# Kernel tuning notes

Measured on AMD Instinct MI355X. Metric: run time of the kernel, lower is better.

## Reference

```python
import jax, jax.numpy as jnp
import numpy as np

N_MLPS = 256
N_BLOCKS = 8
TCODE = 13
IN_F = 3
HID = 128
OUT_F = 1
B = 256
NPTS = 2048
K = 256  # 8-bit codebook
OMEGA = 30.0

# per-layer (fan_in, fan_out) for weight reconstruction
LAYER_SHAPES = [(IN_F + TCODE, HID), (HID, HID), (HID, HID), (HID, OUT_F)]


def setup_inputs() -> dict:
    key = jax.random.key(0)
    ks = jax.random.split(key, 20)
    inp = {
        "x": jax.random.uniform(ks[0], (B, NPTS, IN_F), jnp.float32, -1.0, 1.0),
        "mlp_idx": jax.random.randint(ks[1], (B,), 0, N_MLPS, jnp.int32),
        "block_idx": jax.random.randint(ks[2], (B,), 0, N_BLOCKS, jnp.int32),
        "latent_table": jax.random.normal(ks[3], (N_MLPS, N_BLOCKS, TCODE), jnp.float32),
    }
    for l, (fi, fo) in enumerate(LAYER_SHAPES):
        bound = 1.0 / np.sqrt(fi)
        inp[f"centroids_l{l}"] = jax.random.uniform(ks[4 + 3 * l], (K,), jnp.float32, -bound, bound)
        inp[f"labels_l{l}"] = jax.random.randint(ks[5 + 3 * l], (N_MLPS * fi * fo,), 0, K, jnp.int32)
        inp[f"bias_l{l}"] = jax.random.uniform(ks[6 + 3 * l], (N_MLPS, 1, fo), jnp.float32, -bound, bound)
    return inp


def _layer(h, idx, centroids, labels, bias, fi, fo, apply_sin):
    # codebook dequant: weight.view(-1)[:] = centroids[labels]
    weight = centroids[labels].reshape(N_MLPS, fi, fo)
    # indexed bmm: torch.bmm(x, weight[indices]) + bias[indices]
    out = jnp.einsum("bni,bio->bno", h, weight[idx]) + bias[idx]
    return jnp.sin(OMEGA * out) if apply_sin else out


def reference(x, mlp_idx, block_idx, latent_table,
              centroids_l0, labels_l0, bias_l0,
              centroids_l1, labels_l1, bias_l1,
              centroids_l2, labels_l2, bias_l2,
              centroids_l3, labels_l3, bias_l3):
    # gather per-sample latent code and concat with coords
    z = latent_table[mlp_idx, block_idx]                      # [B, TCODE]
    h = jnp.concatenate(
        [x, jnp.broadcast_to(z[:, None, :], (x.shape[0], x.shape[1], TCODE))], axis=-1)
    cs = [centroids_l0, centroids_l1, centroids_l2, centroids_l3]
    ls = [labels_l0, labels_l1, labels_l2, labels_l3]
    bs = [bias_l0, bias_l1, bias_l2, bias_l3]
    for l, (fi, fo) in enumerate(LAYER_SHAPES):
        h = _layer(h, mlp_idx, cs[l], ls[l], bs[l], fi, fo, apply_sin=(l < len(LAYER_SHAPES) - 1))
    return h
```

## Files before the change

### kernel.cpp

```cpp
#include <hip/hip_runtime.h>


typedef unsigned int u32;
typedef unsigned short u16;
typedef __bf16 v8bf  __attribute__((ext_vector_type(8)));
typedef __bf16 v2bf  __attribute__((ext_vector_type(2)));
typedef float  v16f  __attribute__((ext_vector_type(16)));
typedef float  v2f   __attribute__((ext_vector_type(2)));
typedef u32    v4u   __attribute__((ext_vector_type(4)));
typedef u32    v2u   __attribute__((ext_vector_type(2)));

#define MFMA(a, b, c) __builtin_amdgcn_mfma_f32_32x32x16_bf16(a, b, c, 0, 0, 0)

#define HSTRIDE 136
#define OMEGA_S 4.774648292756860f

__device__ __forceinline__ float sinrev(float rev) {
    return __builtin_amdgcn_sinf(__builtin_amdgcn_fractf(rev));
}

__device__ __forceinline__ u32 pack2(float c) {
    __bf16 b0 = (__bf16)c;
    float  f0 = (float)b0;
    __bf16 b1 = (__bf16)(c - f0);
    return (u32)__builtin_bit_cast(u16, b0) |
           ((u32)__builtin_bit_cast(u16, b1) << 16);
}

__device__ __forceinline__ void pk2(float s0, float s1, u32& lo, u32& hi) {
    v2f s; s[0] = s0; s[1] = s1;
    v2bf l = __builtin_convertvector(s, v2bf);
    u32 lov = __builtin_bit_cast(u32, l);
    v2f lf;
    lf[0] = __builtin_bit_cast(float, lov << 16);
    lf[1] = __builtin_bit_cast(float, lov & 0xffff0000u);
    v2f r = s - lf;
    v2bf h = __builtin_convertvector(r, v2bf);
    lo = lov;
    hi = __builtin_bit_cast(u32, h);
}

__device__ __forceinline__ u32 pklo(float s0, float s1) {
    v2f s; s[0] = s0; s[1] = s1;
    v2bf l = __builtin_convertvector(s, v2bf);
    return __builtin_bit_cast(u32, l);
}

#define PLO(a, b) __builtin_amdgcn_perm((a), (b), 0x05040100u)
#define PHI(a, b) __builtin_amdgcn_perm((a), (b), 0x07060302u)

__global__ __launch_bounds__(512)
void ecnr_dequant(const float* __restrict__ cent0, const int* __restrict__ lab0,
                  const float* __restrict__ cent1, const int* __restrict__ lab1,
                  const float* __restrict__ cent2, const int* __restrict__ lab2,
                  const float* __restrict__ cent3, const int* __restrict__ lab3,
                  const float* __restrict__ bias0, const float* __restrict__ bias1,
                  const float* __restrict__ bias2,
                  u16* __restrict__ wpl1, u16* __restrict__ wpl2,
                  u16* __restrict__ w0pl, u16* __restrict__ w3pl,
                  float* __restrict__ biasc)
{
    __shared__ u32 cpk[512];
    const int t = threadIdx.x;

    if (blockIdx.x < 512) {
        const int m = blockIdx.x >> 1, L = blockIdx.x & 1;
        if (t < 256) cpk[t] = pack2((L ? cent2 : cent1)[t] * OMEGA_S);
        __syncthreads();
        const int* lab = (L ? lab2 : lab1) + (size_t)m * 16384;
        u16* base = (L ? wpl2 : wpl1) + (size_t)m * 32768;
        #pragma unroll
        for (int i = 0; i < 4; ++i) {
            const int id = i * 512 + t;
            const int n = id & 127, c = id >> 7;
            u32 g[8];
            #pragma unroll
            for (int j = 0; j < 8; ++j) g[j] = cpk[lab[(8 * c + j) * 128 + n]];
            v4u lo, hi;
            #pragma unroll
            for (int r = 0; r < 4; ++r) {
                lo[r] = PLO(g[2 * r + 1], g[2 * r]);
                hi[r] = PHI(g[2 * r + 1], g[2 * r]);
            }
            *(v4u*)(base + c * 1024 + n * 8)         = lo;
            *(v4u*)(base + 16384 + c * 1024 + n * 8) = hi;
        }
    } else {
        const int m = blockIdx.x - 512;
        if (t < 256) cpk[t] = pack2(cent0[t] * OMEGA_S);
        else         cpk[t] = pack2(cent3[t - 256]);
        __syncthreads();
        if (t < 256) {
            const int n = t & 127, c = t >> 7;
            const int* lab = lab0 + (size_t)m * 2048;
            u32 g[8];
            #pragma unroll
            for (int j = 0; j < 8; ++j) g[j] = cpk[lab[(8 * c + j) * 128 + n]];
            v4u lo, hi;
            #pragma unroll
            for (int r = 0; r < 4; ++r) {
                lo[r] = PLO(g[2 * r + 1], g[2 * r]);
                hi[r] = PHI(g[2 * r + 1], g[2 * r]);
            }
            u16* b0 = w0pl + (size_t)m * 4096;
            *(v4u*)(b0 + c * 1024 + n * 8)        = lo;
            *(v4u*)(b0 + 2048 + c * 1024 + n * 8) = hi;
        } else if (t < 384) {
            const int kk = t - 256;
            const u32 u = cpk[256 + lab3[(size_t)m * 128 + kk]];
            w3pl[(size_t)m * 256 + kk]       = (u16)u;
            w3pl[(size_t)m * 256 + 128 + kk] = (u16)(u >> 16);
        }
        if (t < 384) {
            const int li = t >> 7, kk = t & 127;
            const float* bsrc = (li == 0) ? bias0 : (li == 1) ? bias1 : bias2;
            biasc[(size_t)m * 384 + t] = bsrc[m * 128 + kk] * OMEGA_S;
        }
    }
}

__global__ __launch_bounds__(512, 8)
void ecnr_fwd(const float* __restrict__ x,
              const int*   __restrict__ mlp_idx,
              const int*   __restrict__ block_idx,
              const float* __restrict__ latent,
              const float* __restrict__ bias3,
              const u16* __restrict__ wpl1, const u16* __restrict__ wpl2,
              const u16* __restrict__ w0pl, const u16* __restrict__ w3pl,
              const float* __restrict__ biasc,
              float* __restrict__ out)
{
    __shared__ __attribute__((aligned(16))) u16   Hlo[64 * HSTRIDE];
    __shared__ __attribute__((aligned(16))) u16   Hhi[64 * HSTRIDE];
    __shared__ __attribute__((aligned(16))) float biasS[2 * 128];
    __shared__ __attribute__((aligned(16))) float red[2 * 128];

    const int g    = blockIdx.x;
    const int b    = ((g >> 8) << 3) | (g & 7);
    const int p0   = ((g >> 3) & 31) * 64;
    const int m    = mlp_idx[b];

    const int t  = threadIdx.x;
    const int l  = t & 63, w = t >> 6;
    const int q  = l >> 5, ln = l & 31;
    const int pt = w & 1, nt = w >> 1;
    const int mrow = pt * 32 + ln;
    const int nn   = nt * 32 + ln;
    const int bidx = nt * 32 + 4 * q;

    const float* bc = biasc + (size_t)m * 384;
    if (t < 128) {
        biasS[t]       = bc[128 + t];
        biasS[128 + t] = bc[256 + t];
    }
    const float* xp = x + (size_t)(b * 2048 + p0 + mrow) * 3;
    const float xv0 = xp[0], xv1 = xp[1], xv2 = xp[2];
    const u16* w0p = w0pl + (size_t)m * 4096 + q * 1024 + nn * 8;
    const v4u w0lo = *(const v4u*)(w0p);
    const v4u w0hi = *(const v4u*)(w0p + 2048);
    float4 b0f[4];
    #pragma unroll
    for (int gg = 0; gg < 4; ++gg)
        b0f[gg] = *(const float4*)(bc + bidx + 8 * gg);
    const float* zp = latent + ((size_t)m * 8 + block_idx[b]) * 13;
    float zr[8];
    #pragma unroll
    for (int j = 0; j < 8; ++j) zr[j] = zp[q * 5 + j];

    u16* lop = Hlo + mrow * HSTRIDE + nt * 32 + 4 * q;
    u16* hip = Hhi + mrow * HSTRIDE + nt * 32 + 4 * q;

    {
        float fin[8];
        if (q == 0) {
            fin[0] = xv0; fin[1] = xv1; fin[2] = xv2;
            #pragma unroll
            for (int j = 0; j < 5; ++j) fin[3 + j] = zr[j];
        } else {
            #pragma unroll
            for (int j = 0; j < 8; ++j) fin[j] = zr[j];
        }
        v4u il, ih;
        #pragma unroll
        for (int r = 0; r < 4; ++r) {
            u32 plo, phi;
            pk2(fin[2 * r], fin[2 * r + 1], plo, phi);
            il[r] = plo; ih[r] = phi;
        }
        const v8bf inlo = __builtin_bit_cast(v8bf, il);
        const v8bf inhi = __builtin_bit_cast(v8bf, ih);
        const v8bf wl = __builtin_bit_cast(v8bf, w0lo);
        const v8bf wh = __builtin_bit_cast(v8bf, w0hi);
        v16f acc;
        #pragma unroll
        for (int gg = 0; gg < 4; ++gg) {
            acc[4 * gg] = b0f[gg].x; acc[4 * gg + 1] = b0f[gg].y;
            acc[4 * gg + 2] = b0f[gg].z; acc[4 * gg + 3] = b0f[gg].w;
        }
        acc = MFMA(wl, inlo, acc);
        acc = MFMA(wl, inhi, acc);
        acc = MFMA(wh, inlo, acc);
        #pragma unroll
        for (int gg = 0; gg < 4; ++gg) {
            const float s0 = sinrev(acc[4 * gg + 0]);
            const float s1 = sinrev(acc[4 * gg + 1]);
            const float s2 = sinrev(acc[4 * gg + 2]);
            const float s3 = sinrev(acc[4 * gg + 3]);
            u32 l0, h0, l1, h1;
            pk2(s0, s1, l0, h0);
            pk2(s2, s3, l1, h1);
            v2u lov, hiv;
            lov[0] = l0; lov[1] = l1;
            hiv[0] = h0; hiv[1] = h1;
            *(v2u*)(lop + 8 * gg) = lov;
            *(v2u*)(hip + 8 * gg) = hiv;
        }
    }
    __syncthreads();

    const u16* HLO = Hlo + mrow * HSTRIDE + q * 8;
    const u16* HHI = Hhi + mrow * HSTRIDE + q * 8;
    #pragma unroll 1
    for (int L = 0; L < 2; ++L) {
        const u16* Wb = (L ? wpl2 : wpl1) + (size_t)m * 32768 + q * 1024 + nn * 8;
        v16f acc;
        #pragma unroll
        for (int gg = 0; gg < 4; ++gg) {
            const float4 bv = *(const float4*)&biasS[L * 128 + bidx + 8 * gg];
            acc[4 * gg] = bv.x; acc[4 * gg + 1] = bv.y;
            acc[4 * gg + 2] = bv.z; acc[4 * gg + 3] = bv.w;
        }
        v4u wl8[8];
        #pragma unroll
        for (int kc = 0; kc < 8; ++kc)
            wl8[kc] = *(const v4u*)(Wb + kc * 2048);
        #pragma unroll
        for (int kc = 0; kc < 8; ++kc) {
            const v4u whv = *(const v4u*)(Wb + kc * 2048 + 16384);
            const v8bf hlo = *(const v8bf*)(HLO + kc * 16);
            const v8bf hhi = *(const v8bf*)(HHI + kc * 16);
            acc = MFMA(__builtin_bit_cast(v8bf, wl8[kc]), hlo, acc);
            acc = MFMA(__builtin_bit_cast(v8bf, wl8[kc]), hhi, acc);
            acc = MFMA(__builtin_bit_cast(v8bf, whv), hlo, acc);
        }
        __syncthreads();
        if (L == 0) {
            #pragma unroll
            for (int gg = 0; gg < 4; ++gg) {
                const float s0 = sinrev(acc[4 * gg + 0]);
                const float s1 = sinrev(acc[4 * gg + 1]);
                const float s2 = sinrev(acc[4 * gg + 2]);
                const float s3 = sinrev(acc[4 * gg + 3]);
                u32 l0, h0, l1, h1;
                pk2(s0, s1, l0, h0);
                pk2(s2, s3, l1, h1);
                v2u lov, hiv;
                lov[0] = l0; lov[1] = l1;
                hiv[0] = h0; hiv[1] = h1;
                *(v2u*)(lop + 8 * gg) = lov;
                *(v2u*)(hip + 8 * gg) = hiv;
            }
        } else {
            #pragma unroll
            for (int gg = 0; gg < 4; ++gg) {
                const float s0 = sinrev(acc[4 * gg + 0]);
                const float s1 = sinrev(acc[4 * gg + 1]);
                const float s2 = sinrev(acc[4 * gg + 2]);
                const float s3 = sinrev(acc[4 * gg + 3]);
                v2u lov;
                lov[0] = pklo(s0, s1);
                lov[1] = pklo(s2, s3);
                *(v2u*)(lop + 8 * gg) = lov;
            }
        }
        __syncthreads();
    }

    {
        const u16* w3b = w3pl + (size_t)m * 256 + nt * 32 + q * 8;
        const u16* h3l = Hlo + mrow * HSTRIDE + nt * 32 + q * 8;
        v16f a3;
        #pragma unroll
        for (int r = 0; r < 16; ++r) a3[r] = 0.0f;
        #pragma unroll
        for (int kc = 0; kc < 2; ++kc) {
            const v8bf wl = *(const v8bf*)(w3b + kc * 16);
            const v8bf wh = *(const v8bf*)(w3b + 128 + kc * 16);
            const v8bf hl = *(const v8bf*)(h3l + kc * 16);
            a3 = MFMA(wl, hl, a3);
            a3 = MFMA(wh, hl, a3);
        }
        if (q == 0) red[pt * 128 + nt * 32 + ln] = a3[0];
    }
    __syncthreads();

    if (t < 64) {
        const int rp = (t >> 5) * 128, rl = t & 31;
        const float o = bias3[m]
            + red[rp + rl] + red[rp + 32 + rl]
            + red[rp + 64 + rl] + red[rp + 96 + rl];
        out[(size_t)b * 2048 + p0 + t] = o;
    }
}

extern "C" void kernel_launch(void* const* d_in, const int* in_sizes, int n_in,
                              void* d_out, int out_size, void* d_ws, size_t ws_size,
                              hipStream_t stream) {
    (void)in_sizes; (void)n_in; (void)out_size; (void)ws_size;
    u16*   wpl1  = (u16*)d_ws;
    u16*   wpl2  = wpl1 + (size_t)256 * 32768;
    u16*   w0pl  = wpl2 + (size_t)256 * 32768;
    u16*   w3pl  = w0pl + (size_t)256 * 4096;
    float* biasc = (float*)(w3pl + (size_t)256 * 256);

    ecnr_dequant<<<768, 512, 0, stream>>>(
        (const float*)d_in[4],  (const int*)d_in[5],
        (const float*)d_in[7],  (const int*)d_in[8],
        (const float*)d_in[10], (const int*)d_in[11],
        (const float*)d_in[13], (const int*)d_in[14],
        (const float*)d_in[6],  (const float*)d_in[9], (const float*)d_in[12],
        wpl1, wpl2, w0pl, w3pl, biasc);

    ecnr_fwd<<<8192, 512, 0, stream>>>(
        (const float*)d_in[0], (const int*)d_in[1], (const int*)d_in[2],
        (const float*)d_in[3],
        (const float*)d_in[15],
        wpl1, wpl2, w0pl, w3pl, biasc,
        (float*)d_out);
}
```

Before: 241.3 us.

## Halve block to 4 waves, each computing two 32-point tiles per weight load

Each wave now handles both 32-row point tiles (A and B) for its 32 output columns, so every weight fragment loaded from global memory feeds two MFMA chains instead of one. The block shrinks from 512 to 256 threads, which halves redundant weight loads per block and interleaves two independent accumulator chains to hide MFMA latency. s_setprio is raised around the MFMA bursts. The cost is roughly double the accumulator and input registers per thread and fewer waves per block, which may reduce occupancy.

```diff
diff --git a/kernel.cpp b/kernel.cpp
--- a/kernel.cpp
+++ b/kernel.cpp
@@ -119,7 +119,42 @@
     }
 }
 
-__global__ __launch_bounds__(512, 8)
+
+#define EPI_FULL(ACC, LOP, HIP)                                   \
+    do {                                                          \
+        _Pragma("unroll")                                         \
+        for (int gg = 0; gg < 4; ++gg) {                          \
+            const float s0 = sinrev((ACC)[4 * gg + 0]);           \
+            const float s1 = sinrev((ACC)[4 * gg + 1]);           \
+            const float s2 = sinrev((ACC)[4 * gg + 2]);           \
+            const float s3 = sinrev((ACC)[4 * gg + 3]);           \
+            u32 l0, h0, l1, h1;                                   \
+            pk2(s0, s1, l0, h0);                                  \
+            pk2(s2, s3, l1, h1);                                  \
+            v2u lov, hiv;                                         \
+            lov[0] = l0; lov[1] = l1;                             \
+            hiv[0] = h0; hiv[1] = h1;                             \
+            *(v2u*)((LOP) + 8 * gg) = lov;                        \
+            *(v2u*)((HIP) + 8 * gg) = hiv;                        \
+        }                                                         \
+    } while (0)
+
+#define EPI_LO(ACC, LOP)                                          \
+    do {                                                          \
+        _Pragma("unroll")                                         \
+        for (int gg = 0; gg < 4; ++gg) {                          \
+            const float s0 = sinrev((ACC)[4 * gg + 0]);           \
+            const float s1 = sinrev((ACC)[4 * gg + 1]);           \
+            const float s2 = sinrev((ACC)[4 * gg + 2]);           \
+            const float s3 = sinrev((ACC)[4 * gg + 3]);           \
+            v2u lov;                                              \
+            lov[0] = pklo(s0, s1);                                \
+            lov[1] = pklo(s2, s3);                                \
+            *(v2u*)((LOP) + 8 * gg) = lov;                        \
+        }                                                         \
+    } while (0)
+
+__global__ __launch_bounds__(256, 4)
 void ecnr_fwd(const float* __restrict__ x,
               const int*   __restrict__ mlp_idx,
               const int*   __restrict__ block_idx,
@@ -141,10 +176,8 @@
     const int m    = mlp_idx[b];
 
     const int t  = threadIdx.x;
-    const int l  = t & 63, w = t >> 6;
+    const int l  = t & 63, nt = t >> 6;
     const int q  = l >> 5, ln = l & 31;
-    const int pt = w & 1, nt = w >> 1;
-    const int mrow = pt * 32 + ln;
     const int nn   = nt * 32 + ln;
     const int bidx = nt * 32 + 4 * q;
 
@@ -153,8 +186,9 @@
         biasS[t]       = bc[128 + t];
         biasS[128 + t] = bc[256 + t];
     }
-    const float* xp = x + (size_t)(b * 2048 + p0 + mrow) * 3;
-    const float xv0 = xp[0], xv1 = xp[1], xv2 = xp[2];
+    const float* xpA = x + (size_t)(b * 2048 + p0 + ln) * 3;
+    const float xA0 = xpA[0], xA1 = xpA[1], xA2 = xpA[2];
+    const float xB0 = xpA[96], xB1 = xpA[97], xB2 = xpA[98];
     const u16* w0p = w0pl + (size_t)m * 4096 + q * 1024 + nn * 8;
     const v4u w0lo = *(const v4u*)(w0p);
     const v4u w0hi = *(const v4u*)(w0p + 2048);
@@ -167,68 +201,70 @@
     #pragma unroll
     for (int j = 0; j < 8; ++j) zr[j] = zp[q * 5 + j];
 
-    u16* lop = Hlo + mrow * HSTRIDE + nt * 32 + 4 * q;
-    u16* hip = Hhi + mrow * HSTRIDE + nt * 32 + 4 * q;
+    u16* lopA = Hlo + ln * HSTRIDE + nt * 32 + 4 * q;
+    u16* hipA = Hhi + ln * HSTRIDE + nt * 32 + 4 * q;
+    u16* lopB = lopA + 32 * HSTRIDE;
+    u16* hipB = hipA + 32 * HSTRIDE;
 
     {
-        float fin[8];
+        float finA[8], finB[8];
         if (q == 0) {
-            fin[0] = xv0; fin[1] = xv1; fin[2] = xv2;
-            #pragma unroll
-            for (int j = 0; j < 5; ++j) fin[3 + j] = zr[j];
+            finA[0] = xA0; finA[1] = xA1; finA[2] = xA2;
+            finB[0] = xB0; finB[1] = xB1; finB[2] = xB2;
+            #pragma unroll
+            for (int j = 0; j < 5; ++j) { finA[3 + j] = zr[j]; finB[3 + j] = zr[j]; }
         } else {
             #pragma unroll
-            for (int j = 0; j < 8; ++j) fin[j] = zr[j];
-        }
-        v4u il, ih;
+            for (int j = 0; j < 8; ++j) { finA[j] = zr[j]; finB[j] = zr[j]; }
+        }
+        v4u ilA, ihA, ilB, ihB;
         #pragma unroll
         for (int r = 0; r < 4; ++r) {
             u32 plo, phi;
-            pk2(fin[2 * r], fin[2 * r + 1], plo, phi);
-            il[r] = plo; ih[r] = phi;
-        }
-        const v8bf inlo = __builtin_bit_cast(v8bf, il);
-        const v8bf inhi = __builtin_bit_cast(v8bf, ih);
+            pk2(finA[2 * r], finA[2 * r + 1], plo, phi);
+            ilA[r] = plo; ihA[r] = phi;
+            pk2(finB[2 * r], finB[2 * r + 1], plo, phi);
+            ilB[r] = plo; ihB[r] = phi;
+        }
+        const v8bf inloA = __builtin_bit_cast(v8bf, ilA);
+        const v8bf inhiA = __builtin_bit_cast(v8bf, ihA);
+        const v8bf inloB = __builtin_bit_cast(v8bf, ilB);
+        const v8bf inhiB = __builtin_bit_cast(v8bf, ihB);
         const v8bf wl = __builtin_bit_cast(v8bf, w0lo);
         const v8bf wh = __builtin_bit_cast(v8bf, w0hi);
-        v16f acc;
+        v16f accA, accB;
         #pragma unroll
         for (int gg = 0; gg < 4; ++gg) {
-            acc[4 * gg] = b0f[gg].x; acc[4 * gg + 1] = b0f[gg].y;
-            acc[4 * gg + 2] = b0f[gg].z; acc[4 * gg + 3] = b0f[gg].w;
-        }
-        acc = MFMA(wl, inlo, acc);
-        acc = MFMA(wl, inhi, acc);
-        acc = MFMA(wh, inlo, acc);
-        #pragma unroll
-        for (int gg = 0; gg < 4; ++gg) {
-            const float s0 = sinrev(acc[4 * gg + 0]);
-            const float s1 = sinrev(acc[4 * gg + 1]);
-            const float s2 = sinrev(acc[4 * gg + 2]);
-            const float s3 = sinrev(acc[4 * gg + 3]);
-            u32 l0, h0, l1, h1;
-            pk2(s0, s1, l0, h0);
-            pk2(s2, s3, l1, h1);
-            v2u lov, hiv;
-            lov[0] = l0; lov[1] = l1;
-            hiv[0] = h0; hiv[1] = h1;
-            *(v2u*)(lop + 8 * gg) = lov;
-            *(v2u*)(hip + 8 * gg) = hiv;
-        }
+            accA[4 * gg] = b0f[gg].x; accA[4 * gg + 1] = b0f[gg].y;
+            accA[4 * gg + 2] = b0f[gg].z; accA[4 * gg + 3] = b0f[gg].w;
+            accB[4 * gg] = b0f[gg].x; accB[4 * gg + 1] = b0f[gg].y;
+            accB[4 * gg + 2] = b0f[gg].z; accB[4 * gg + 3] = b0f[gg].w;
+        }
+        __builtin_amdgcn_s_setprio(1);
+        accA = MFMA(wl, inloA, accA); accB = MFMA(wl, inloB, accB);
+        accA = MFMA(wl, inhiA, accA); accB = MFMA(wl, inhiB, accB);
+        accA = MFMA(wh, inloA, accA); accB = MFMA(wh, inloB, accB);
+        __builtin_amdgcn_s_setprio(0);
+        EPI_FULL(accA, lopA, hipA);
+        EPI_FULL(accB, lopB, hipB);
     }
     __syncthreads();
 
-    const u16* HLO = Hlo + mrow * HSTRIDE + q * 8;
-    const u16* HHI = Hhi + mrow * HSTRIDE + q * 8;
+    const u16* HLA = Hlo + ln * HSTRIDE + q * 8;
+    const u16* HHA = Hhi + ln * HSTRIDE + q * 8;
+    const u16* HLB = HLA + 32 * HSTRIDE;
+    const u16* HHB = HHA + 32 * HSTRIDE;
     #pragma unroll 1
     for (int L = 0; L < 2; ++L) {
         const u16* Wb = (L ? wpl2 : wpl1) + (size_t)m * 32768 + q * 1024 + nn * 8;
-        v16f acc;
+        v16f accA, accB;
         #pragma unroll
         for (int gg = 0; gg < 4; ++gg) {
             const float4 bv = *(const float4*)&biasS[L * 128 + bidx + 8 * gg];
-            acc[4 * gg] = bv.x; acc[4 * gg + 1] = bv.y;
-            acc[4 * gg + 2] = bv.z; acc[4 * gg + 3] = bv.w;
+            accA[4 * gg] = bv.x; accA[4 * gg + 1] = bv.y;
+            accA[4 * gg + 2] = bv.z; accA[4 * gg + 3] = bv.w;
+            accB[4 * gg] = bv.x; accB[4 * gg + 1] = bv.y;
+            accB[4 * gg + 2] = bv.z; accB[4 * gg + 3] = bv.w;
         }
         v4u wl8[8];
         #pragma unroll
@@ -237,60 +273,51 @@
         #pragma unroll
         for (int kc = 0; kc < 8; ++kc) {
             const v4u whv = *(const v4u*)(Wb + kc * 2048 + 16384);
-            const v8bf hlo = *(const v8bf*)(HLO + kc * 16);
-            const v8bf hhi = *(const v8bf*)(HHI + kc * 16);
-            acc = MFMA(__builtin_bit_cast(v8bf, wl8[kc]), hlo, acc);
-            acc = MFMA(__builtin_bit_cast(v8bf, wl8[kc]), hhi, acc);
-            acc = MFMA(__builtin_bit_cast(v8bf, whv), hlo, acc);
+            const v8bf hloA = *(const v8bf*)(HLA + kc * 16);
+            const v8bf hhiA = *(const v8bf*)(HHA + kc * 16);
+            const v8bf hloB = *(const v8bf*)(HLB + kc * 16);
+            const v8bf hhiB = *(const v8bf*)(HHB + kc * 16);
+            const v8bf wlv = __builtin_bit_cast(v8bf, wl8[kc]);
+            const v8bf whb = __builtin_bit_cast(v8bf, whv);
+            __builtin_amdgcn_s_setprio(1);
+            accA = MFMA(wlv, hloA, accA); accB = MFMA(wlv, hloB, accB);
+            accA = MFMA(wlv, hhiA, accA); accB = MFMA(wlv, hhiB, accB);
+            accA = MFMA(whb, hloA, accA); accB = MFMA(whb, hloB, accB);
+            __builtin_amdgcn_s_setprio(0);
         }
         __syncthreads();
         if (L == 0) {
-            #pragma unroll
-            for (int gg = 0; gg < 4; ++gg) {
-                const float s0 = sinrev(acc[4 * gg + 0]);
-                const float s1 = sinrev(acc[4 * gg + 1]);
-                const float s2 = sinrev(acc[4 * gg + 2]);
-                const float s3 = sinrev(acc[4 * gg + 3]);
-                u32 l0, h0, l1, h1;
-                pk2(s0, s1, l0, h0);
-                pk2(s2, s3, l1, h1);
-                v2u lov, hiv;
-                lov[0] = l0; lov[1] = l1;
-                hiv[0] = h0; hiv[1] = h1;
-                *(v2u*)(lop + 8 * gg) = lov;
-                *(v2u*)(hip + 8 * gg) = hiv;
-            }
+            EPI_FULL(accA, lopA, hipA);
+            EPI_FULL(accB, lopB, hipB);
         } else {
-            #pragma unroll
-            for (int gg = 0; gg < 4; ++gg) {
-                const float s0 = sinrev(acc[4 * gg + 0]);
-                const float s1 = sinrev(acc[4 * gg + 1]);
-                const float s2 = sinrev(acc[4 * gg + 2]);
-                const float s3 = sinrev(acc[4 * gg + 3]);
-                v2u lov;
-                lov[0] = pklo(s0, s1);
-                lov[1] = pklo(s2, s3);
-                *(v2u*)(lop + 8 * gg) = lov;
-            }
+            EPI_LO(accA, lopA);
+            EPI_LO(accB, lopB);
         }
         __syncthreads();
     }
 
     {
         const u16* w3b = w3pl + (size_t)m * 256 + nt * 32 + q * 8;
-        const u16* h3l = Hlo + mrow * HSTRIDE + nt * 32 + q * 8;
-        v16f a3;
-        #pragma unroll
-        for (int r = 0; r < 16; ++r) a3[r] = 0.0f;
+        const u16* h3A = Hlo + ln * HSTRIDE + nt * 32 + q * 8;
+        const u16* h3B = h3A + 32 * HSTRIDE;
+        v16f aA, aB;
+        #pragma unroll
+        for (int r = 0; r < 16; ++r) { aA[r] = 0.0f; aB[r] = 0.0f; }
         #pragma unroll
         for (int kc = 0; kc < 2; ++kc) {
             const v8bf wl = *(const v8bf*)(w3b + kc * 16);
             const v8bf wh = *(const v8bf*)(w3b + 128 + kc * 16);
-            const v8bf hl = *(const v8bf*)(h3l + kc * 16);
-            a3 = MFMA(wl, hl, a3);
-            a3 = MFMA(wh, hl, a3);
-        }
-        if (q == 0) red[pt * 128 + nt * 32 + ln] = a3[0];
+            const v8bf hA = *(const v8bf*)(h3A + kc * 16);
+            const v8bf hB = *(const v8bf*)(h3B + kc * 16);
+            __builtin_amdgcn_s_setprio(1);
+            aA = MFMA(wl, hA, aA); aB = MFMA(wl, hB, aB);
+            aA = MFMA(wh, hA, aA); aB = MFMA(wh, hB, aB);
+            __builtin_amdgcn_s_setprio(0);
+        }
+        if (q == 0) {
+            red[nt * 32 + ln]       = aA[0];
+            red[128 + nt * 32 + ln] = aB[0];
+        }
     }
     __syncthreads();
 
@@ -321,7 +348,7 @@
         (const float*)d_in[6],  (const float*)d_in[9], (const float*)d_in[12],
         wpl1, wpl2, w0pl, w3pl, biasc);
 
-    ecnr_fwd<<<8192, 512, 0, stream>>>(
+    ecnr_fwd<<<8192, 256, 0, stream>>>(
         (const float*)d_in[0], (const int*)d_in[1], (const int*)d_in[2],
         (const float*)d_in[3],
         (const float*)d_in[15],
```

Result: faster. 222.6 us (-7.7%).
